# Performance work log

Hardware: AMD Instinct MI355X
Metric: run time of the kernel (lower is better)

The kernel has to match this reference:

```python
import jax, jax.numpy as jnp
import numpy as np

N_NODES = 50000
N_EDGES = 800000
D_IN = 128
D_OUT = 128


def setup_inputs() -> dict:
    key = jax.random.key(0)
    k1, k2, k3, k4, k5, k6 = jax.random.split(key, 6)
    x = jax.random.normal(k1, (N_NODES, D_IN), dtype=jnp.float32)
    weight = jax.random.normal(k2, (D_IN, D_OUT), dtype=jnp.float32)
    bias = jax.random.normal(k3, (D_OUT,), dtype=jnp.float32)
    adj_row = jax.random.randint(k4, (N_EDGES,), 0, N_NODES, dtype=jnp.int64)
    adj_col = jax.random.randint(k5, (N_EDGES,), 0, N_NODES, dtype=jnp.int64)
    adj_val = jax.random.uniform(k6, (N_EDGES,), dtype=jnp.float32)
    return {"x": x, "weight": weight, "bias": bias,
            "adj_row": adj_row, "adj_col": adj_col, "adj_val": adj_val}


def reference(x, weight, bias, adj_row, adj_col, adj_val):
    # support = x @ W  -- dense GEMM [N, D_in] x [D_in, D_out]
    support = jnp.matmul(x, weight)
    # spmm(adj, support): out[i] = sum_e adj_val[e] * support[adj_col[e]] for adj_row[e]==i
    messages = support[adj_col] * adj_val[:, None]          # [E, D_out]
    output = jax.ops.segment_sum(messages, adj_row, num_segments=x.shape[0])
    return output + bias
```

## Files before the change

### kernel.cpp

```cpp
#include <hip/hip_runtime.h>

#define D 128
#define ELL_CAP 64
#define EPT 8

typedef __attribute__((ext_vector_type(8))) short short8;
typedef __attribute__((ext_vector_type(4))) float floatx4;
typedef unsigned int uint;
typedef unsigned short ushort;

__device__ inline short f2bf(float f) {
  unsigned u = __float_as_uint(f);
  u += 0x7FFF + ((u >> 16) & 1);
  return (short)(u >> 16);
}

__global__ __launch_bounds__(256) void gemm_scatter_kernel(
    const float* __restrict__ x, const float* __restrict__ w,
    ushort* __restrict__ support, int n_nodes, int gemm_blocks,
    const int* __restrict__ adj_row, const int* __restrict__ adj_col,
    const float* __restrict__ adj_val, int* __restrict__ cnt,
    uint* __restrict__ ell, int n_edges, int range_size) {
  __shared__ short sWA[4 * 8 * 64 * 8];
  const int tid = threadIdx.x;

  if ((int)blockIdx.x < gemm_blocks) {
    const float4* w4 = (const float4*)w;
    for (int t = tid; t < D * D / 4; t += 256) {
      float4 v = w4[t];
      int k = t >> 5;
      int m0 = (t & 31) * 4;
      int kt = k >> 5, quad = (k >> 3) & 3, j = k & 7;
      float vv[4] = {v.x, v.y, v.z, v.w};
#pragma unroll
      for (int u = 0; u < 4; ++u) {
        int m = m0 + u;
        int mt = m >> 4, nid = m & 15;
        sWA[((kt * 8 + mt) * 64 + quad * 16 + nid) * 8 + j] = f2bf(vv[u]);
      }
    }
    __syncthreads();

    const int wid = tid >> 6;
    const int lane = tid & 63;
    const int quad = lane >> 4;
    const int node = blockIdx.x * 64 + wid * 16 + (lane & 15);
    const bool ok = (node < n_nodes);

    floatx4 acc[8];
#pragma unroll
    for (int mt = 0; mt < 8; ++mt) acc[mt] = (floatx4){0.f, 0.f, 0.f, 0.f};

#pragma unroll
    for (int kt = 0; kt < 4; ++kt) {
      short8 b = (short8){0, 0, 0, 0, 0, 0, 0, 0};
      if (ok) {
        const float4 v0 = *(const float4*)&x[(size_t)node * D + kt * 32 + quad * 8];
        const float4 v1 = *(const float4*)&x[(size_t)node * D + kt * 32 + quad * 8 + 4];
        b = (short8){f2bf(v0.x), f2bf(v0.y), f2bf(v0.z), f2bf(v0.w),
                     f2bf(v1.x), f2bf(v1.y), f2bf(v1.z), f2bf(v1.w)};
      }
#pragma unroll
      for (int mt = 0; mt < 8; ++mt) {
        short8 a = *(const short8*)&sWA[((kt * 8 + mt) * 64 + lane) * 8];
        acc[mt] = __builtin_amdgcn_mfma_f32_16x16x32_bf16(a, b, acc[mt], 0, 0, 0);
      }
    }

    if (ok) {
#pragma unroll
      for (int mt = 0; mt < 8; ++mt) {
        uint lo = ((uint)(ushort)f2bf(acc[mt][1]) << 16) | (ushort)f2bf(acc[mt][0]);
        uint hi = ((uint)(ushort)f2bf(acc[mt][3]) << 16) | (ushort)f2bf(acc[mt][2]);
        *(uint2*)&support[(size_t)node * D + mt * 16 + quad * 4] = make_uint2(lo, hi);
      }
    }
  } else {
    const int b = blockIdx.x - gemm_blocks;
    const int g = b & 7;
    const int c = b >> 3;
    const int lo = g * range_size, hi = lo + range_size;
    const int base = c * (256 * EPT) + tid * EPT;

    if (base + EPT <= n_edges) {
      int4 r0 = *(const int4*)&adj_row[base];
      int4 r1 = *(const int4*)&adj_row[base + 4];
      int4 c0 = *(const int4*)&adj_col[base];
      int4 c1 = *(const int4*)&adj_col[base + 4];
      float4 v0 = *(const float4*)&adj_val[base];
      float4 v1 = *(const float4*)&adj_val[base + 4];
      int rr[EPT] = {r0.x, r0.y, r0.z, r0.w, r1.x, r1.y, r1.z, r1.w};
      int cc[EPT] = {c0.x, c0.y, c0.z, c0.w, c1.x, c1.y, c1.z, c1.w};
      float vv[EPT] = {v0.x, v0.y, v0.z, v0.w, v1.x, v1.y, v1.z, v1.w};
#pragma unroll
      for (int u = 0; u < EPT; ++u) {
        int r = rr[u];
        if (r >= lo && r < hi) {
          int pos = atomicAdd(&cnt[r], 1);
          if (pos < ELL_CAP)
            ell[(size_t)r * ELL_CAP + pos] = ((uint)cc[u] << 16) | (ushort)f2bf(vv[u]);
        }
      }
    } else {
      for (int u = 0; u < EPT; ++u) {
        int e = base + u;
        if (e >= n_edges) break;
        int r = adj_row[e];
        if (r >= lo && r < hi) {
          int pos = atomicAdd(&cnt[r], 1);
          if (pos < ELL_CAP)
            ell[(size_t)r * ELL_CAP + pos] = ((uint)adj_col[e] << 16) | (ushort)f2bf(adj_val[e]);
        }
      }
    }
  }
}

__global__ __launch_bounds__(256) void spmm_ell_kernel(const int* __restrict__ cnt,
                                                       const uint* __restrict__ ell,
                                                       const uint* __restrict__ sup,
                                                       const float* __restrict__ bias,
                                                       float* __restrict__ out,
                                                       int n_rows) {
  int wave = (int)((blockIdx.x * 256 + threadIdx.x) >> 6);
  int lane = threadIdx.x & 63;
  if (wave >= n_rows) return;
  const int r = wave;
  int n = cnt[r];
  if (n > ELL_CAP) n = ELL_CAP;
  uint ent = 0;
  if (lane < n) ent = ell[(size_t)r * ELL_CAP + lane];
  float ax = 0.f, ay = 0.f;
  const int m = (n + 7) & ~7;
  for (int j = 0; j < m; j += 8) {
    uint e[8];
    uint s[8];
#pragma unroll
    for (int u = 0; u < 8; ++u) e[u] = __shfl(ent, j + u);
#pragma unroll
    for (int u = 0; u < 8; ++u) s[u] = sup[(size_t)(e[u] >> 16) * 64 + lane];
#pragma unroll
    for (int u = 0; u < 8; ++u) {
      float wv = __uint_as_float(e[u] << 16);
      ax = fmaf(wv, __uint_as_float(s[u] << 16), ax);
      ay = fmaf(wv, __uint_as_float(s[u] & 0xffff0000u), ay);
    }
  }
  float2 b = *(const float2*)&bias[lane * 2];
  *(float2*)&out[(size_t)r * D + lane * 2] = make_float2(b.x + ax, b.y + ay);
}

extern "C" void kernel_launch(void* const* d_in, const int* in_sizes, int n_in,
                              void* d_out, int out_size, void* d_ws, size_t ws_size,
                              hipStream_t stream) {
  const float* x       = (const float*)d_in[0];
  const float* w       = (const float*)d_in[1];
  const float* bias    = (const float*)d_in[2];
  const int*   adj_row = (const int*)d_in[3];
  const int*   adj_col = (const int*)d_in[4];
  const float* adj_val = (const float*)d_in[5];

  const int n_nodes = in_sizes[0] / D;
  const int n_edges = in_sizes[3];
  float* out = (float*)d_out;

  char* ws = (char*)d_ws;
  ushort* support = (ushort*)ws; ws += ((size_t)n_nodes * D * 2 + 15) & ~15ull;
  int*    row_cnt = (int*)ws;    ws += ((size_t)n_nodes * 4 + 15) & ~15ull;
  uint*   ell     = (uint*)ws;   ws += (size_t)n_nodes * ELL_CAP * 4;

  hipMemsetAsync(row_cnt, 0, (size_t)n_nodes * 4, stream);

  const int gemm_blocks = (n_nodes + 63) / 64;
  const int range_size = (n_nodes + 7) / 8;
  const int chunks = (n_edges + 256 * EPT - 1) / (256 * EPT);
  gemm_scatter_kernel<<<gemm_blocks + chunks * 8, 256, 0, stream>>>(
      x, w, support, n_nodes, gemm_blocks,
      adj_row, adj_col, adj_val, row_cnt, ell, n_edges, range_size);

  int spmm_blocks = (n_nodes + 3) / 4;
  spmm_ell_kernel<<<spmm_blocks, 256, 0, stream>>>(row_cnt, ell, (const uint*)support,
                                                   bias, out, n_nodes);
}
```

Measured before the change: 157.3 us.

## Schedule scatter blocks first and use nontemporal loads/stores for streaming data

Reorders the fused kernel so the atomic-heavy edge scatter blocks are dispatched before the GEMM blocks, letting the latency-bound scatter start early and the GEMM fill in behind it. It switches the one-pass streams (edge arrays, x rows, final output) to nontemporal loads and stores so they do not evict reused data such as support and the ELL buffer from cache. The weight staging is rewritten so each thread builds a whole 8-element fragment and writes it to shared memory as one vector store, at the cost of strided global reads of the weight matrix.

```diff
diff --git a/kernel.cpp b/kernel.cpp
--- a/kernel.cpp
+++ b/kernel.cpp
@@ -6,6 +6,9 @@
 
 typedef __attribute__((ext_vector_type(8))) short short8;
 typedef __attribute__((ext_vector_type(4))) float floatx4;
+typedef __attribute__((ext_vector_type(4))) float fltx4;
+typedef __attribute__((ext_vector_type(2))) float fltx2;
+typedef __attribute__((ext_vector_type(4))) int intx4;
 typedef unsigned int uint;
 typedef unsigned short ushort;
 
@@ -17,78 +20,27 @@
 
 __global__ __launch_bounds__(256) void gemm_scatter_kernel(
     const float* __restrict__ x, const float* __restrict__ w,
-    ushort* __restrict__ support, int n_nodes, int gemm_blocks,
+    ushort* __restrict__ support, int n_nodes, int scatter_blocks,
     const int* __restrict__ adj_row, const int* __restrict__ adj_col,
     const float* __restrict__ adj_val, int* __restrict__ cnt,
     uint* __restrict__ ell, int n_edges, int range_size) {
   __shared__ short sWA[4 * 8 * 64 * 8];
   const int tid = threadIdx.x;
 
-  if ((int)blockIdx.x < gemm_blocks) {
-    const float4* w4 = (const float4*)w;
-    for (int t = tid; t < D * D / 4; t += 256) {
-      float4 v = w4[t];
-      int k = t >> 5;
-      int m0 = (t & 31) * 4;
-      int kt = k >> 5, quad = (k >> 3) & 3, j = k & 7;
-      float vv[4] = {v.x, v.y, v.z, v.w};
-#pragma unroll
-      for (int u = 0; u < 4; ++u) {
-        int m = m0 + u;
-        int mt = m >> 4, nid = m & 15;
-        sWA[((kt * 8 + mt) * 64 + quad * 16 + nid) * 8 + j] = f2bf(vv[u]);
-      }
-    }
-    __syncthreads();
-
-    const int wid = tid >> 6;
-    const int lane = tid & 63;
-    const int quad = lane >> 4;
-    const int node = blockIdx.x * 64 + wid * 16 + (lane & 15);
-    const bool ok = (node < n_nodes);
-
-    floatx4 acc[8];
-#pragma unroll
-    for (int mt = 0; mt < 8; ++mt) acc[mt] = (floatx4){0.f, 0.f, 0.f, 0.f};
-
-#pragma unroll
-    for (int kt = 0; kt < 4; ++kt) {
-      short8 b = (short8){0, 0, 0, 0, 0, 0, 0, 0};
-      if (ok) {
-        const float4 v0 = *(const float4*)&x[(size_t)node * D + kt * 32 + quad * 8];
-        const float4 v1 = *(const float4*)&x[(size_t)node * D + kt * 32 + quad * 8 + 4];
-        b = (short8){f2bf(v0.x), f2bf(v0.y), f2bf(v0.z), f2bf(v0.w),
-                     f2bf(v1.x), f2bf(v1.y), f2bf(v1.z), f2bf(v1.w)};
-      }
-#pragma unroll
-      for (int mt = 0; mt < 8; ++mt) {
-        short8 a = *(const short8*)&sWA[((kt * 8 + mt) * 64 + lane) * 8];
-        acc[mt] = __builtin_amdgcn_mfma_f32_16x16x32_bf16(a, b, acc[mt], 0, 0, 0);
-      }
-    }
-
-    if (ok) {
-#pragma unroll
-      for (int mt = 0; mt < 8; ++mt) {
-        uint lo = ((uint)(ushort)f2bf(acc[mt][1]) << 16) | (ushort)f2bf(acc[mt][0]);
-        uint hi = ((uint)(ushort)f2bf(acc[mt][3]) << 16) | (ushort)f2bf(acc[mt][2]);
-        *(uint2*)&support[(size_t)node * D + mt * 16 + quad * 4] = make_uint2(lo, hi);
-      }
-    }
-  } else {
-    const int b = blockIdx.x - gemm_blocks;
+  if ((int)blockIdx.x < scatter_blocks) {
+    const int b = blockIdx.x;
     const int g = b & 7;
     const int c = b >> 3;
     const int lo = g * range_size, hi = lo + range_size;
     const int base = c * (256 * EPT) + tid * EPT;
 
     if (base + EPT <= n_edges) {
-      int4 r0 = *(const int4*)&adj_row[base];
-      int4 r1 = *(const int4*)&adj_row[base + 4];
-      int4 c0 = *(const int4*)&adj_col[base];
-      int4 c1 = *(const int4*)&adj_col[base + 4];
-      float4 v0 = *(const float4*)&adj_val[base];
-      float4 v1 = *(const float4*)&adj_val[base + 4];
+      intx4 r0 = __builtin_nontemporal_load((const intx4*)&adj_row[base]);
+      intx4 r1 = __builtin_nontemporal_load((const intx4*)&adj_row[base + 4]);
+      intx4 c0 = __builtin_nontemporal_load((const intx4*)&adj_col[base]);
+      intx4 c1 = __builtin_nontemporal_load((const intx4*)&adj_col[base + 4]);
+      fltx4 v0 = __builtin_nontemporal_load((const fltx4*)&adj_val[base]);
+      fltx4 v1 = __builtin_nontemporal_load((const fltx4*)&adj_val[base + 4]);
       int rr[EPT] = {r0.x, r0.y, r0.z, r0.w, r1.x, r1.y, r1.z, r1.w};
       int cc[EPT] = {c0.x, c0.y, c0.z, c0.w, c1.x, c1.y, c1.z, c1.w};
       float vv[EPT] = {v0.x, v0.y, v0.z, v0.w, v1.x, v1.y, v1.z, v1.w};
@@ -111,6 +63,56 @@
           if (pos < ELL_CAP)
             ell[(size_t)r * ELL_CAP + pos] = ((uint)adj_col[e] << 16) | (ushort)f2bf(adj_val[e]);
         }
+      }
+    }
+  } else {
+    const int bx = blockIdx.x - scatter_blocks;
+
+    for (int s = tid; s < 2048; s += 256) {
+      int ktmt = s >> 6, ls = s & 63;
+      int kb = (ktmt >> 3) * 32 + (ls >> 4) * 8;
+      int m = (ktmt & 7) * 16 + (ls & 15);
+      short8 frag;
+#pragma unroll
+      for (int j = 0; j < 8; ++j) frag[j] = f2bf(w[(kb + j) * D + m]);
+      *(short8*)&sWA[s * 8] = frag;
+    }
+    __syncthreads();
+
+    const int wid = tid >> 6;
+    const int lane = tid & 63;
+    const int quad = lane >> 4;
+    const int node = bx * 64 + wid * 16 + (lane & 15);
+    const bool ok = (node < n_nodes);
+
+    floatx4 acc[8];
+#pragma unroll
+    for (int mt = 0; mt < 8; ++mt) acc[mt] = (floatx4){0.f, 0.f, 0.f, 0.f};
+
+#pragma unroll
+    for (int kt = 0; kt < 4; ++kt) {
+      short8 bfr = (short8){0, 0, 0, 0, 0, 0, 0, 0};
+      if (ok) {
+        fltx4 v0 = __builtin_nontemporal_load(
+            (const fltx4*)&x[(size_t)node * D + kt * 32 + quad * 8]);
+        fltx4 v1 = __builtin_nontemporal_load(
+            (const fltx4*)&x[(size_t)node * D + kt * 32 + quad * 8 + 4]);
+        bfr = (short8){f2bf(v0.x), f2bf(v0.y), f2bf(v0.z), f2bf(v0.w),
+                       f2bf(v1.x), f2bf(v1.y), f2bf(v1.z), f2bf(v1.w)};
+      }
+#pragma unroll
+      for (int mt = 0; mt < 8; ++mt) {
+        short8 a = *(const short8*)&sWA[((kt * 8 + mt) * 64 + lane) * 8];
+        acc[mt] = __builtin_amdgcn_mfma_f32_16x16x32_bf16(a, bfr, acc[mt], 0, 0, 0);
+      }
+    }
+
+    if (ok) {
+#pragma unroll
+      for (int mt = 0; mt < 8; ++mt) {
+        uint lo = ((uint)(ushort)f2bf(acc[mt][1]) << 16) | (ushort)f2bf(acc[mt][0]);
+        uint hi = ((uint)(ushort)f2bf(acc[mt][3]) << 16) | (ushort)f2bf(acc[mt][2]);
+        *(uint2*)&support[(size_t)node * D + mt * 16 + quad * 4] = make_uint2(lo, hi);
       }
     }
   }
@@ -147,7 +149,8 @@
     }
   }
   float2 b = *(const float2*)&bias[lane * 2];
-  *(float2*)&out[(size_t)r * D + lane * 2] = make_float2(b.x + ax, b.y + ay);
+  fltx2 o = (fltx2){b.x + ax, b.y + ay};
+  __builtin_nontemporal_store(o, (fltx2*)&out[(size_t)r * D + lane * 2]);
 }
 
 extern "C" void kernel_launch(void* const* d_in, const int* in_sizes, int n_in,
@@ -174,8 +177,9 @@
   const int gemm_blocks = (n_nodes + 63) / 64;
   const int range_size = (n_nodes + 7) / 8;
   const int chunks = (n_edges + 256 * EPT - 1) / (256 * EPT);
-  gemm_scatter_kernel<<<gemm_blocks + chunks * 8, 256, 0, stream>>>(
-      x, w, support, n_nodes, gemm_blocks,
+  const int scatter_blocks = chunks * 8;
+  gemm_scatter_kernel<<<scatter_blocks + gemm_blocks, 256, 0, stream>>>(
+      x, w, support, n_nodes, scatter_blocks,
       adj_row, adj_col, adj_val, row_cnt, ell, n_edges, range_size);
 
   int spmm_blocks = (n_nodes + 3) / 4;
```

Result: slower. 169.2 us (+7.6%).

## Process two rows per wavefront in SpMM and rewrite weight-fragment staging

Applied to the files above, without the earlier changes.

The SpMM kernel now maps two output rows to each 64-lane wave, with each half-wave handling one row and each lane loading 8 bytes (4 bf16 values) of a support row. This halves the wave count and widens the per-lane gathers. Shuffle sources are adjusted so each half reads its own row's ELL entries, and the loop runs to the longer of the two rows. The GEMM weight staging also changes: each thread builds a whole 8-element bf16 fragment and writes it to LDS in one store, replacing scattered 2-byte stores; the global reads of w become strided as a result.

```diff
diff --git a/kernel.cpp b/kernel.cpp
--- a/kernel.cpp
+++ b/kernel.cpp
@@ -25,19 +25,14 @@
   const int tid = threadIdx.x;
 
   if ((int)blockIdx.x < gemm_blocks) {
-    const float4* w4 = (const float4*)w;
-    for (int t = tid; t < D * D / 4; t += 256) {
-      float4 v = w4[t];
-      int k = t >> 5;
-      int m0 = (t & 31) * 4;
-      int kt = k >> 5, quad = (k >> 3) & 3, j = k & 7;
-      float vv[4] = {v.x, v.y, v.z, v.w};
-#pragma unroll
-      for (int u = 0; u < 4; ++u) {
-        int m = m0 + u;
-        int mt = m >> 4, nid = m & 15;
-        sWA[((kt * 8 + mt) * 64 + quad * 16 + nid) * 8 + j] = f2bf(vv[u]);
-      }
+    for (int s = tid; s < 2048; s += 256) {
+      int ktmt = s >> 6, ls = s & 63;
+      int kb = (ktmt >> 3) * 32 + (ls >> 4) * 8;
+      int m = (ktmt & 7) * 16 + (ls & 15);
+      short8 frag;
+#pragma unroll
+      for (int j = 0; j < 8; ++j) frag[j] = f2bf(w[(kb + j) * D + m]);
+      *(short8*)&sWA[s * 8] = frag;
     }
     __syncthreads();
 
@@ -53,17 +48,17 @@
 
 #pragma unroll
     for (int kt = 0; kt < 4; ++kt) {
-      short8 b = (short8){0, 0, 0, 0, 0, 0, 0, 0};
+      short8 bfr = (short8){0, 0, 0, 0, 0, 0, 0, 0};
       if (ok) {
         const float4 v0 = *(const float4*)&x[(size_t)node * D + kt * 32 + quad * 8];
         const float4 v1 = *(const float4*)&x[(size_t)node * D + kt * 32 + quad * 8 + 4];
-        b = (short8){f2bf(v0.x), f2bf(v0.y), f2bf(v0.z), f2bf(v0.w),
-                     f2bf(v1.x), f2bf(v1.y), f2bf(v1.z), f2bf(v1.w)};
+        bfr = (short8){f2bf(v0.x), f2bf(v0.y), f2bf(v0.z), f2bf(v0.w),
+                       f2bf(v1.x), f2bf(v1.y), f2bf(v1.z), f2bf(v1.w)};
       }
 #pragma unroll
       for (int mt = 0; mt < 8; ++mt) {
         short8 a = *(const short8*)&sWA[((kt * 8 + mt) * 64 + lane) * 8];
-        acc[mt] = __builtin_amdgcn_mfma_f32_16x16x32_bf16(a, b, acc[mt], 0, 0, 0);
+        acc[mt] = __builtin_amdgcn_mfma_f32_16x16x32_bf16(a, bfr, acc[mt], 0, 0, 0);
       }
     }
 
@@ -122,32 +117,53 @@
                                                        const float* __restrict__ bias,
                                                        float* __restrict__ out,
                                                        int n_rows) {
-  int wave = (int)((blockIdx.x * 256 + threadIdx.x) >> 6);
-  int lane = threadIdx.x & 63;
-  if (wave >= n_rows) return;
-  const int r = wave;
-  int n = cnt[r];
+  const int wave = (int)((blockIdx.x * 256 + threadIdx.x) >> 6);
+  const int lane = threadIdx.x & 63;
+  const int half = lane >> 5;
+  const int hl = lane & 31;
+  const int r = wave * 2 + half;
+  if (wave * 2 >= n_rows) return;
+
+  int n = 0;
+  if (r < n_rows) n = cnt[r];
   if (n > ELL_CAP) n = ELL_CAP;
-  uint ent = 0;
-  if (lane < n) ent = ell[(size_t)r * ELL_CAP + lane];
-  float ax = 0.f, ay = 0.f;
-  const int m = (n + 7) & ~7;
+  uint ent0 = 0, ent1 = 0;
+  if (hl < n) ent0 = ell[(size_t)r * ELL_CAP + hl];
+  if (hl + 32 < n) ent1 = ell[(size_t)r * ELL_CAP + 32 + hl];
+
+  int nmax = n;
+  int no = __shfl_xor(nmax, 32);
+  if (no > nmax) nmax = no;
+  const int m = (nmax + 7) & ~7;
+
+  float a0 = 0.f, a1 = 0.f, a2 = 0.f, a3 = 0.f;
   for (int j = 0; j < m; j += 8) {
     uint e[8];
-    uint s[8];
-#pragma unroll
-    for (int u = 0; u < 8; ++u) e[u] = __shfl(ent, j + u);
-#pragma unroll
-    for (int u = 0; u < 8; ++u) s[u] = sup[(size_t)(e[u] >> 16) * 64 + lane];
+    uint2 s[8];
+#pragma unroll
+    for (int u = 0; u < 8; ++u) {
+      int jj = j + u;
+      int src = (half << 5) + (jj & 31);
+      e[u] = __shfl(jj < 32 ? ent0 : ent1, src);
+    }
+#pragma unroll
+    for (int u = 0; u < 8; ++u)
+      s[u] = *(const uint2*)&sup[(size_t)(e[u] >> 16) * 64 + hl * 2];
 #pragma unroll
     for (int u = 0; u < 8; ++u) {
       float wv = __uint_as_float(e[u] << 16);
-      ax = fmaf(wv, __uint_as_float(s[u] << 16), ax);
-      ay = fmaf(wv, __uint_as_float(s[u] & 0xffff0000u), ay);
+      a0 = fmaf(wv, __uint_as_float(s[u].x << 16), a0);
+      a1 = fmaf(wv, __uint_as_float(s[u].x & 0xffff0000u), a1);
+      a2 = fmaf(wv, __uint_as_float(s[u].y << 16), a2);
+      a3 = fmaf(wv, __uint_as_float(s[u].y & 0xffff0000u), a3);
     }
   }
-  float2 b = *(const float2*)&bias[lane * 2];
-  *(float2*)&out[(size_t)r * D + lane * 2] = make_float2(b.x + ax, b.y + ay);
+
+  if (r < n_rows) {
+    float4 b = *(const float4*)&bias[hl * 4];
+    *(float4*)&out[(size_t)r * D + hl * 4] =
+        make_float4(b.x + a0, b.y + a1, b.z + a2, b.w + a3);
+  }
 }
 
 extern "C" void kernel_launch(void* const* d_in, const int* in_sizes, int n_in,
@@ -178,7 +194,8 @@
       x, w, support, n_nodes, gemm_blocks,
       adj_row, adj_col, adj_val, row_cnt, ell, n_edges, range_size);
 
-  int spmm_blocks = (n_nodes + 3) / 4;
+  int waves = (n_nodes + 1) / 2;
+  int spmm_blocks = (waves + 3) / 4;
   spmm_ell_kernel<<<spmm_blocks, 256, 0, stream>>>(row_cnt, ell, (const uint*)support,
                                                    bias, out, n_nodes);
 }
```

Result: no change. 155.9 us (-0.9%).
